# Kernel optimization log

Hardware: AMD Instinct MI355X
Metric: run time of the kernel (lower is better)

Reference implementation:

```python
import jax, jax.numpy as jnp
import numpy as np

N = 50000        # nodes
E = 800000       # edges (before self-loops)
IN_DIM = 128
OUT_DIM = 128
HEADS = 4
HEAD_DIM = OUT_DIM // HEADS
NEG_SLOPE = 0.2  # GATv2Conv default negative_slope
LN_EPS = 1e-5


def setup_inputs() -> dict:
    key = jax.random.key(0)
    ks = jax.random.split(key, 6)
    def glorot(k, shape, fan):
        return jax.random.normal(k, shape, jnp.float32) * (1.0 / np.sqrt(fan))
    x = jax.random.normal(ks[0], (N, IN_DIM), jnp.float32)
    edge_index = jax.random.randint(ks[1], (2, E), 0, N, dtype=jnp.int32)
    W_l = glorot(ks[2], (IN_DIM, OUT_DIM), IN_DIM)   # lin_l (source/message transform)
    W_r = glorot(ks[3], (IN_DIM, OUT_DIM), IN_DIM)   # lin_r (target transform)
    att = glorot(ks[4], (HEADS, HEAD_DIM), HEAD_DIM)  # per-head attention vector a
    bias = jnp.zeros((OUT_DIM,), jnp.float32)
    gamma = jnp.ones((OUT_DIM,), jnp.float32)
    beta = jnp.zeros((OUT_DIM,), jnp.float32)
    return {"x": x, "edge_index": edge_index, "W_l": W_l, "W_r": W_r,
            "att": att, "bias": bias, "gamma": gamma, "beta": beta}


def reference(x, edge_index, W_l, W_r, att, bias, gamma, beta):
    # --- GATv2Conv (PyG defaults: add_self_loops=True, share_weights=False) ---
    loop = jnp.arange(N, dtype=edge_index.dtype)
    src = jnp.concatenate([edge_index[0], loop])  # message sources j
    dst = jnp.concatenate([edge_index[1], loop])  # message targets i

    xl = (x @ W_l).reshape(N, HEADS, HEAD_DIM)  # source-side features
    xr = (x @ W_r).reshape(N, HEADS, HEAD_DIM)  # target-side features

    h = xl[src] + xr[dst]                                  # [E+N, H, D]
    h = jnp.where(h > 0, h, NEG_SLOPE * h)                 # LeakyReLU
    logits = jnp.einsum('ehd,hd->eh', h, att)              # [E+N, H]

    # segment softmax over incoming edges of each target node
    m = jax.ops.segment_max(logits, dst, num_segments=N)   # [N, H]
    p = jnp.exp(logits - m[dst])
    s = jax.ops.segment_sum(p, dst, num_segments=N)        # [N, H]
    alpha = p / s[dst]                                     # [E+N, H]

    out = jax.ops.segment_sum(alpha[:, :, None] * xl[src], dst, num_segments=N)
    out = out.reshape(N, OUT_DIM) + bias                   # concat heads + bias

    # --- ELU + LayerNorm ---
    out = jax.nn.elu(out)
    mu = jnp.mean(out, axis=-1, keepdims=True)
    var = jnp.var(out, axis=-1, keepdims=True)
    out = (out - mu) / jnp.sqrt(var + LN_EPS) * gamma + beta
    return out
```

## Files before the change

### kernel.cpp

```cpp
#include <hip/hip_runtime.h>

#define IN_DIM   128
#define OUT_DIM  128
#define HEADS    4
#define HEAD_DIM 32
#define NEG_SLOPE 0.2f
#define LN_EPS    1e-5f
#define CAP      64
#define CAP_SH   6
#define NPART    8

typedef __bf16 bf16x8 __attribute__((ext_vector_type(8)));
typedef float  f32x4  __attribute__((ext_vector_type(4)));

__device__ __forceinline__ unsigned short f2bf(float f) {
    unsigned u = __float_as_uint(f);
    u += 0x7fffu + ((u >> 16) & 1u);
    return (unsigned short)(u >> 16);
}

__device__ __forceinline__ void unpack8(uint4 u, float* f) {
    f[0] = __uint_as_float(u.x << 16); f[1] = __uint_as_float(u.x & 0xffff0000u);
    f[2] = __uint_as_float(u.y << 16); f[3] = __uint_as_float(u.y & 0xffff0000u);
    f[4] = __uint_as_float(u.z << 16); f[5] = __uint_as_float(u.z & 0xffff0000u);
    f[6] = __uint_as_float(u.w << 16); f[7] = __uint_as_float(u.w & 0xffff0000u);
}

__global__ void prep0(const float* __restrict__ Wl,
                      const float* __restrict__ Wr,
                      unsigned short* __restrict__ wpack,
                      int* __restrict__ cnt, int N) {
    const int tid = blockIdx.x * 256 + threadIdx.x;
    for (int i = tid; i < N; i += 4096) cnt[i] = 0;

    const int lane = tid & 63;
    const int ks   = (tid >> 6) & 3;
    const int t    = tid >> 8;
    const int nt   = t & 7, half = t >> 3;
    const int n    = nt * 16 + (lane & 15);
    const int k0   = ks * 32 + (lane >> 4) * 8;
    const float* W = half ? Wr : Wl;
    union { unsigned short s[8]; uint4 q; } u;
    #pragma unroll
    for (int j = 0; j < 8; ++j) u.s[j] = f2bf(W[(k0 + j) * OUT_DIM + n]);
    ((uint4*)wpack)[tid] = u.q;
}

__global__ void fill_part(const int* __restrict__ ei, int E, int N, int PART,
                          int* __restrict__ cnt,
                          unsigned short* __restrict__ csr16) {
    const int p  = blockIdx.x & (NPART - 1);
    const int b  = blockIdx.x >> 3;
    const int lo = p * PART;
    const int ET = E + N;
    const int stride = (gridDim.x >> 3) * 256;
    for (int e = b * 256 + threadIdx.x; e < ET; e += stride) {
        int src, dst;
        if (e < E) { dst = ei[E + e]; src = ei[e]; }
        else       { dst = src = e - E; }
        if ((unsigned)(dst - lo) < (unsigned)PART) {
            int pos = atomicAdd(&cnt[dst], 1);
            if (pos < CAP) csr16[(dst << CAP_SH) + pos] = (unsigned short)src;
        }
    }
}

__global__ void gemm_mfma(const float* __restrict__ x,
                          const unsigned short* __restrict__ wpack,
                          unsigned short* __restrict__ xl,
                          unsigned short* __restrict__ xr,
                          int N) {
    const int wv     = threadIdx.x >> 6;
    const int lane   = threadIdx.x & 63;
    const int rowgrp = wv & 1, half = wv >> 1;
    const int r0     = blockIdx.x * 32 + rowgrp * 16;
    const int m      = lane & 15, quad = lane >> 4;
    const int r      = r0 + m;
    unsigned short* out = half ? xr : xl;
    const uint4* wp = (const uint4*)wpack;

    f32x4 acc[8];
    #pragma unroll
    for (int nt = 0; nt < 8; ++nt) acc[nt] = (f32x4){0.f, 0.f, 0.f, 0.f};

    #pragma unroll
    for (int ks = 0; ks < 4; ++ks) {
        union { unsigned short s[8]; bf16x8 v; } af;
        if (r < N) {
            const float4* xp = (const float4*)(x + (size_t)r * IN_DIM + ks * 32 + quad * 8);
            float4 f0 = xp[0];
            float4 f1 = xp[1];
            af.s[0] = f2bf(f0.x); af.s[1] = f2bf(f0.y);
            af.s[2] = f2bf(f0.z); af.s[3] = f2bf(f0.w);
            af.s[4] = f2bf(f1.x); af.s[5] = f2bf(f1.y);
            af.s[6] = f2bf(f1.z); af.s[7] = f2bf(f1.w);
        } else {
            #pragma unroll
            for (int j = 0; j < 8; ++j) af.s[j] = 0;
        }
        #pragma unroll
        for (int nt = 0; nt < 8; ++nt) {
            union { uint4 q; bf16x8 v; } bf_;
            bf_.q = wp[((half * 8 + nt) * 4 + ks) * 64 + lane];
            acc[nt] = __builtin_amdgcn_mfma_f32_16x16x32_bf16(af.v, bf_.v, acc[nt], 0, 0, 0);
        }
    }

    #pragma unroll
    for (int nt = 0; nt < 8; ++nt) {
        #pragma unroll
        for (int i = 0; i < 4; ++i) {
            int gr = r0 + quad * 4 + i;
            if (gr < N) out[(size_t)gr * OUT_DIM + nt * 16 + m] = f2bf(acc[nt][i]);
        }
    }
}

__global__ void aggregate(const int* __restrict__ cnt,
                          const unsigned short* __restrict__ csr16,
                          const uint4* __restrict__ xlq,
                          const uint4* __restrict__ xrq,
                          const float* __restrict__ att,
                          const float* __restrict__ bias,
                          const float* __restrict__ gamma,
                          const float* __restrict__ beta,
                          float* __restrict__ out, int N) {
    const int node = (int)((blockIdx.x * (size_t)blockDim.x + threadIdx.x) >> 6);
    const int lane = threadIdx.x & 63;
    if (node >= N) return;
    const int slot = lane >> 4;
    const int sl   = lane & 15;

    int deg = cnt[node];
    deg = (deg > CAP) ? CAP : deg;
    const int beg = node << CAP_SH;

    float r[8], a[8];
    unpack8(xrq[(size_t)node * 16 + sl], r);
    const float4 af0 = ((const float4*)att)[2 * sl];
    const float4 af1 = ((const float4*)att)[2 * sl + 1];
    a[0] = af0.x; a[1] = af0.y; a[2] = af0.z; a[3] = af0.w;
    a[4] = af1.x; a[5] = af1.y; a[6] = af1.z; a[7] = af1.w;

    float sden = 0.f;
    float acc[8];
    #pragma unroll
    for (int j = 0; j < 8; ++j) acc[j] = 0.f;

    const int sh = (slot & 1) << 4;
    for (int k = 0; k < deg; k += 8) {
        const uint4 cs = *(const uint4*)(csr16 + beg + k);
        const int id0 = (int)((((slot & 2) ? cs.y : cs.x) >> sh) & 0xffffu);
        const int id1 = (int)((((slot & 2) ? cs.w : cs.z) >> sh) & 0xffffu);
        const uint4 u0 = xlq[(size_t)id0 * 16 + sl];
        const uint4 u1 = xlq[(size_t)id1 * 16 + sl];
        float l0[8], l1[8];
        unpack8(u0, l0);
        unpack8(u1, l1);
        float q0 = 0.f, q1 = 0.f;
        #pragma unroll
        for (int j = 0; j < 8; ++j) {
            float v0 = l0[j] + r[j]; v0 = fmaxf(v0, NEG_SLOPE * v0);
            float v1 = l1[j] + r[j]; v1 = fmaxf(v1, NEG_SLOPE * v1);
            q0 = fmaf(v0, a[j], q0);
            q1 = fmaf(v1, a[j], q1);
        }
        q0 += __shfl_xor(q0, 1, 64); q1 += __shfl_xor(q1, 1, 64);
        q0 += __shfl_xor(q0, 2, 64); q1 += __shfl_xor(q1, 2, 64);
        const float pe0 = (k + slot     < deg) ? __expf(q0) : 0.f;
        const float pe1 = (k + 4 + slot < deg) ? __expf(q1) : 0.f;
        sden += pe0 + pe1;
        #pragma unroll
        for (int j = 0; j < 8; ++j)
            acc[j] = fmaf(pe1, l1[j], fmaf(pe0, l0[j], acc[j]));
    }

    #pragma unroll
    for (int o = 16; o <= 32; o <<= 1) {
        sden += __shfl_xor(sden, o, 64);
        #pragma unroll
        for (int j = 0; j < 8; ++j) acc[j] += __shfl_xor(acc[j], o, 64);
    }

    const float inv_s = 1.f / sden;
    const float4 b0 = ((const float4*)bias)[2 * sl];
    const float4 b1 = ((const float4*)bias)[2 * sl + 1];
    float bi[8] = {b0.x, b0.y, b0.z, b0.w, b1.x, b1.y, b1.z, b1.w};
    float v[8];
    float sum = 0.f, ssq = 0.f;
    #pragma unroll
    for (int j = 0; j < 8; ++j) {
        float t = acc[j] * inv_s + bi[j];
        t = (t > 0.f) ? t : (__expf(t) - 1.f);
        v[j] = t;
        sum += t;
        ssq = fmaf(t, t, ssq);
    }
    #pragma unroll
    for (int o = 1; o <= 8; o <<= 1) {
        sum += __shfl_xor(sum, o, 64);
        ssq += __shfl_xor(ssq, o, 64);
    }
    const float mean = sum * (1.f / 128.f);
    const float var  = ssq * (1.f / 128.f) - mean * mean;
    const float inv  = rsqrtf(var + LN_EPS);
    if (slot == 0) {
        const float4 g0 = ((const float4*)gamma)[2 * sl];
        const float4 g1 = ((const float4*)gamma)[2 * sl + 1];
        const float4 t0 = ((const float4*)beta)[2 * sl];
        const float4 t1 = ((const float4*)beta)[2 * sl + 1];
        float4 o0, o1;
        o0.x = (v[0] - mean) * inv * g0.x + t0.x;
        o0.y = (v[1] - mean) * inv * g0.y + t0.y;
        o0.z = (v[2] - mean) * inv * g0.z + t0.z;
        o0.w = (v[3] - mean) * inv * g0.w + t0.w;
        o1.x = (v[4] - mean) * inv * g1.x + t1.x;
        o1.y = (v[5] - mean) * inv * g1.y + t1.y;
        o1.z = (v[6] - mean) * inv * g1.z + t1.z;
        o1.w = (v[7] - mean) * inv * g1.w + t1.w;
        float4* orow = (float4*)(out + (size_t)node * OUT_DIM);
        orow[2 * sl]     = o0;
        orow[2 * sl + 1] = o1;
    }
}

extern "C" void kernel_launch(void* const* d_in, const int* in_sizes, int n_in,
                              void* d_out, int out_size, void* d_ws, size_t ws_size,
                              hipStream_t stream) {
    const float* x     = (const float*)d_in[0];
    const int*   ei    = (const int*)  d_in[1];
    const float* Wl    = (const float*)d_in[2];
    const float* Wr    = (const float*)d_in[3];
    const float* att   = (const float*)d_in[4];
    const float* bias  = (const float*)d_in[5];
    const float* gamma = (const float*)d_in[6];
    const float* beta  = (const float*)d_in[7];
    float* out = (float*)d_out;

    const int N  = in_sizes[0] / IN_DIM;
    const int E  = in_sizes[1] / 2;

    char* ws = (char*)d_ws;
    unsigned short* xl    = (unsigned short*)ws;
    unsigned short* xr    = xl + (size_t)N * OUT_DIM;
    unsigned short* wpack = xr + (size_t)N * OUT_DIM;
    unsigned short* csr16 = wpack + 32768;
    int* cnt = (int*)(csr16 + (size_t)N * CAP);

    const int PART = (N + NPART - 1) / NPART;

    prep0<<<16, 256, 0, stream>>>(Wl, Wr, wpack, cnt, N);

    fill_part<<<1024, 256, 0, stream>>>(ei, E, N, PART, cnt, csr16);

    gemm_mfma<<<(N + 31) / 32, 256, 0, stream>>>(x, wpack, xl, xr, N);

    aggregate<<<(N + 3) / 4, 256, 0, stream>>>(
        cnt, csr16, (const uint4*)xl, (const uint4*)xr,
        att, bias, gamma, beta, out, N);
}
```

Before: 199.4 us.

## Bin edges by destination partition and fuse CSR scatter with GEMM launch

Replaces the partitioned fill kernel, which had every block re-read all edges and filter by destination range, with a binning pass. That pass buckets packed (dst,src) pairs into 8 partitions using shared-memory histograms. A combined kernel then scatters the binned edges into the capped CSR in some blocks and runs the MFMA GEMM in the others, so the two overlap within one launch. The aggregate kernel is also rewritten with float2 packed helpers, likely to encourage packed FP32 math. This adds an extra edge buffer pass and packs node ids into 16 bits, which relies on N fitting in 16 bits.

```diff
diff --git a/kernel.cpp b/kernel.cpp
--- a/kernel.cpp
+++ b/kernel.cpp
@@ -8,7 +8,7 @@
 #define LN_EPS    1e-5f
 #define CAP      64
 #define CAP_SH   6
-#define NPART    8
+#define BIN_EDGES 4096
 
 typedef __bf16 bf16x8 __attribute__((ext_vector_type(8)));
 typedef float  f32x4  __attribute__((ext_vector_type(4)));
@@ -19,11 +19,23 @@
     return (unsigned short)(u >> 16);
 }
 
-__device__ __forceinline__ void unpack8(uint4 u, float* f) {
-    f[0] = __uint_as_float(u.x << 16); f[1] = __uint_as_float(u.x & 0xffff0000u);
-    f[2] = __uint_as_float(u.y << 16); f[3] = __uint_as_float(u.y & 0xffff0000u);
-    f[4] = __uint_as_float(u.z << 16); f[5] = __uint_as_float(u.z & 0xffff0000u);
-    f[6] = __uint_as_float(u.w << 16); f[7] = __uint_as_float(u.w & 0xffff0000u);
+__device__ __forceinline__ float2 bf2up(unsigned u) {
+    return make_float2(__uint_as_float(u << 16), __uint_as_float(u & 0xffff0000u));
+}
+__device__ __forceinline__ float2 pk_add(float2 a, float2 b) {
+    return make_float2(a.x + b.x, a.y + b.y);
+}
+__device__ __forceinline__ float2 pk_max(float2 a, float2 b) {
+    return make_float2(fmaxf(a.x, b.x), fmaxf(a.y, b.y));
+}
+__device__ __forceinline__ float2 pk_muls(float2 a, float s) {
+    return make_float2(a.x * s, a.y * s);
+}
+__device__ __forceinline__ float2 pk_fma(float2 a, float2 b, float2 c) {
+    return make_float2(fmaf(a.x, b.x, c.x), fmaf(a.y, b.y, c.y));
+}
+__device__ __forceinline__ float2 pk_fmas(float s, float2 b, float2 c) {
+    return make_float2(fmaf(s, b.x, c.x), fmaf(s, b.y, c.y));
 }
 
 __global__ void prep0(const float* __restrict__ Wl,
@@ -31,7 +43,7 @@
                       unsigned short* __restrict__ wpack,
                       int* __restrict__ cnt, int N) {
     const int tid = blockIdx.x * 256 + threadIdx.x;
-    for (int i = tid; i < N; i += 4096) cnt[i] = 0;
+    for (int i = tid; i < N + 8; i += 4096) cnt[i] = 0;
 
     const int lane = tid & 63;
     const int ks   = (tid >> 6) & 3;
@@ -46,34 +58,71 @@
     ((uint4*)wpack)[tid] = u.q;
 }
 
-__global__ void fill_part(const int* __restrict__ ei, int E, int N, int PART,
-                          int* __restrict__ cnt,
-                          unsigned short* __restrict__ csr16) {
-    const int p  = blockIdx.x & (NPART - 1);
-    const int b  = blockIdx.x >> 3;
-    const int lo = p * PART;
-    const int ET = E + N;
-    const int stride = (gridDim.x >> 3) * 256;
-    for (int e = b * 256 + threadIdx.x; e < ET; e += stride) {
-        int src, dst;
-        if (e < E) { dst = ei[E + e]; src = ei[e]; }
-        else       { dst = src = e - E; }
-        if ((unsigned)(dst - lo) < (unsigned)PART) {
-            int pos = atomicAdd(&cnt[dst], 1);
+__global__ void bin_edges(const int* __restrict__ ei, int E, int N,
+                          unsigned* __restrict__ buf, int bufstride,
+                          int* __restrict__ pcur) {
+    __shared__ int lhist[8], lbase[8];
+    if (threadIdx.x < 8) lhist[threadIdx.x] = 0;
+    __syncthreads();
+    const int ET  = E + N;
+    const int seg = blockIdx.x * BIN_EDGES;
+    unsigned pr[16], rk[16];
+    #pragma unroll
+    for (int j = 0; j < 16; ++j) {
+        const int e = seg + j * 256 + threadIdx.x;
+        rk[j] = 0xffffffffu;
+        if (e < ET) {
+            int src, dst;
+            if (e < E) { dst = ei[E + e]; src = ei[e]; }
+            else       { dst = src = e - E; }
+            const int p = dst >> 13;
+            pr[j] = ((unsigned)dst << 16) | (unsigned)src;
+            const int r = atomicAdd(&lhist[p], 1);
+            rk[j] = ((unsigned)p << 16) | (unsigned)r;
+        }
+    }
+    __syncthreads();
+    if (threadIdx.x < 8)
+        lbase[threadIdx.x] = atomicAdd(&pcur[threadIdx.x], lhist[threadIdx.x]);
+    __syncthreads();
+    #pragma unroll
+    for (int j = 0; j < 16; ++j) {
+        if (rk[j] != 0xffffffffu) {
+            const int p = rk[j] >> 16, r = rk[j] & 0xffffu;
+            buf[(size_t)p * bufstride + lbase[p] + r] = pr[j];
+        }
+    }
+}
+
+__global__ void scatter_gemm(const unsigned* __restrict__ buf, int bufstride,
+                             const int* __restrict__ pcur,
+                             int* __restrict__ cnt,
+                             unsigned short* __restrict__ csr16,
+                             const float* __restrict__ x,
+                             const unsigned short* __restrict__ wpack,
+                             unsigned short* __restrict__ xl,
+                             unsigned short* __restrict__ xr,
+                             int N) {
+    if (blockIdx.x < 512) {
+        const int p  = blockIdx.x & 7;
+        const int bi = blockIdx.x >> 3;
+        const int pc = pcur[p];
+        const unsigned* b = buf + (size_t)p * bufstride;
+        for (int i = bi * 256 + threadIdx.x; i < pc; i += 64 * 256) {
+            const unsigned pair = b[i];
+            const int dst = (int)(pair >> 16);
+            const int src = (int)(pair & 0xffffu);
+            const int pos = atomicAdd(&cnt[dst], 1);
             if (pos < CAP) csr16[(dst << CAP_SH) + pos] = (unsigned short)src;
         }
-    }
-}
-
-__global__ void gemm_mfma(const float* __restrict__ x,
-                          const unsigned short* __restrict__ wpack,
-                          unsigned short* __restrict__ xl,
-                          unsigned short* __restrict__ xr,
-                          int N) {
+        return;
+    }
+
+    const int bid    = blockIdx.x - 512;
     const int wv     = threadIdx.x >> 6;
     const int lane   = threadIdx.x & 63;
     const int rowgrp = wv & 1, half = wv >> 1;
-    const int r0     = blockIdx.x * 32 + rowgrp * 16;
+    const int r0     = bid * 32 + rowgrp * 16;
     const int m      = lane & 15, quad = lane >> 4;
     const int r      = r0 + m;
     unsigned short* out = half ? xr : xl;
@@ -135,17 +184,16 @@
     deg = (deg > CAP) ? CAP : deg;
     const int beg = node << CAP_SH;
 
-    float r[8], a[8];
-    unpack8(xrq[(size_t)node * 16 + sl], r);
+    const uint4 urq = xrq[(size_t)node * 16 + sl];
+    float2 r2[4] = { bf2up(urq.x), bf2up(urq.y), bf2up(urq.z), bf2up(urq.w) };
     const float4 af0 = ((const float4*)att)[2 * sl];
     const float4 af1 = ((const float4*)att)[2 * sl + 1];
-    a[0] = af0.x; a[1] = af0.y; a[2] = af0.z; a[3] = af0.w;
-    a[4] = af1.x; a[5] = af1.y; a[6] = af1.z; a[7] = af1.w;
+    float2 a2[4] = { make_float2(af0.x, af0.y), make_float2(af0.z, af0.w),
+                     make_float2(af1.x, af1.y), make_float2(af1.z, af1.w) };
 
     float sden = 0.f;
-    float acc[8];
-    #pragma unroll
-    for (int j = 0; j < 8; ++j) acc[j] = 0.f;
+    float2 acc2[4] = { make_float2(0.f, 0.f), make_float2(0.f, 0.f),
+                       make_float2(0.f, 0.f), make_float2(0.f, 0.f) };
 
     const int sh = (slot & 1) << 4;
     for (int k = 0; k < deg; k += 8) {
@@ -154,43 +202,51 @@
         const int id1 = (int)((((slot & 2) ? cs.w : cs.z) >> sh) & 0xffffu);
         const uint4 u0 = xlq[(size_t)id0 * 16 + sl];
         const uint4 u1 = xlq[(size_t)id1 * 16 + sl];
-        float l0[8], l1[8];
-        unpack8(u0, l0);
-        unpack8(u1, l1);
-        float q0 = 0.f, q1 = 0.f;
-        #pragma unroll
-        for (int j = 0; j < 8; ++j) {
-            float v0 = l0[j] + r[j]; v0 = fmaxf(v0, NEG_SLOPE * v0);
-            float v1 = l1[j] + r[j]; v1 = fmaxf(v1, NEG_SLOPE * v1);
-            q0 = fmaf(v0, a[j], q0);
-            q1 = fmaf(v1, a[j], q1);
-        }
+        float2 l0[4] = { bf2up(u0.x), bf2up(u0.y), bf2up(u0.z), bf2up(u0.w) };
+        float2 l1[4] = { bf2up(u1.x), bf2up(u1.y), bf2up(u1.z), bf2up(u1.w) };
+        float2 q0v = make_float2(0.f, 0.f), q1v = make_float2(0.f, 0.f);
+        #pragma unroll
+        for (int j = 0; j < 4; ++j) {
+            float2 v0 = pk_add(l0[j], r2[j]);
+            v0 = pk_max(v0, pk_muls(v0, NEG_SLOPE));
+            q0v = pk_fma(v0, a2[j], q0v);
+            float2 v1 = pk_add(l1[j], r2[j]);
+            v1 = pk_max(v1, pk_muls(v1, NEG_SLOPE));
+            q1v = pk_fma(v1, a2[j], q1v);
+        }
+        float q0 = q0v.x + q0v.y;
+        float q1 = q1v.x + q1v.y;
         q0 += __shfl_xor(q0, 1, 64); q1 += __shfl_xor(q1, 1, 64);
         q0 += __shfl_xor(q0, 2, 64); q1 += __shfl_xor(q1, 2, 64);
         const float pe0 = (k + slot     < deg) ? __expf(q0) : 0.f;
         const float pe1 = (k + 4 + slot < deg) ? __expf(q1) : 0.f;
         sden += pe0 + pe1;
         #pragma unroll
-        for (int j = 0; j < 8; ++j)
-            acc[j] = fmaf(pe1, l1[j], fmaf(pe0, l0[j], acc[j]));
+        for (int j = 0; j < 4; ++j)
+            acc2[j] = pk_fmas(pe1, l1[j], pk_fmas(pe0, l0[j], acc2[j]));
     }
 
     #pragma unroll
     for (int o = 16; o <= 32; o <<= 1) {
         sden += __shfl_xor(sden, o, 64);
         #pragma unroll
-        for (int j = 0; j < 8; ++j) acc[j] += __shfl_xor(acc[j], o, 64);
+        for (int j = 0; j < 4; ++j) {
+            acc2[j].x += __shfl_xor(acc2[j].x, o, 64);
+            acc2[j].y += __shfl_xor(acc2[j].y, o, 64);
+        }
     }
 
     const float inv_s = 1.f / sden;
     const float4 b0 = ((const float4*)bias)[2 * sl];
     const float4 b1 = ((const float4*)bias)[2 * sl + 1];
-    float bi[8] = {b0.x, b0.y, b0.z, b0.w, b1.x, b1.y, b1.z, b1.w};
+    const float bi[8] = {b0.x, b0.y, b0.z, b0.w, b1.x, b1.y, b1.z, b1.w};
+    const float ac[8] = {acc2[0].x, acc2[0].y, acc2[1].x, acc2[1].y,
+                         acc2[2].x, acc2[2].y, acc2[3].x, acc2[3].y};
     float v[8];
     float sum = 0.f, ssq = 0.f;
     #pragma unroll
     for (int j = 0; j < 8; ++j) {
-        float t = acc[j] * inv_s + bi[j];
+        float t = ac[j] * inv_s + bi[j];
         t = (t > 0.f) ? t : (__expf(t) - 1.f);
         v[j] = t;
         sum += t;
@@ -239,6 +295,7 @@
 
     const int N  = in_sizes[0] / IN_DIM;
     const int E  = in_sizes[1] / 2;
+    const int ET = E + N;
 
     char* ws = (char*)d_ws;
     unsigned short* xl    = (unsigned short*)ws;
@@ -246,14 +303,17 @@
     unsigned short* wpack = xr + (size_t)N * OUT_DIM;
     unsigned short* csr16 = wpack + 32768;
     int* cnt = (int*)(csr16 + (size_t)N * CAP);
-
-    const int PART = (N + NPART - 1) / NPART;
+    int* pcur = cnt + N;
+    unsigned* buf = (unsigned*)(pcur + 8);
 
     prep0<<<16, 256, 0, stream>>>(Wl, Wr, wpack, cnt, N);
 
-    fill_part<<<1024, 256, 0, stream>>>(ei, E, N, PART, cnt, csr16);
-
-    gemm_mfma<<<(N + 31) / 32, 256, 0, stream>>>(x, wpack, xl, xr, N);
+    const int binB = (ET + BIN_EDGES - 1) / BIN_EDGES;
+    bin_edges<<<binB, 256, 0, stream>>>(ei, E, N, buf, ET, pcur);
+
+    const int gemmB = (N + 31) / 32;
+    scatter_gemm<<<512 + gemmB, 256, 0, stream>>>(buf, ET, pcur, cnt, csr16,
+                                                  x, wpack, xl, xr, N);
 
     aggregate<<<(N + 3) / 4, 256, 0, stream>>>(
         cnt, csr16, (const uint4*)xl, (const uint4*)xr,
```

After: 196.3 us. Within noise of the previous version (-1.6%).
